# Kernel tuning notes

Measured on AMD Instinct MI355X. Metric: run time of the kernel, lower is better.

## Reference

```python
import jax, jax.numpy as jnp
import numpy as np

N = 100000
E = 1600000
IN = 256
H = 4
C = 64


def setup_inputs() -> dict:
    key = jax.random.key(0)
    k1, k2, k3, k4, k5, k6 = jax.random.split(key, 6)
    x = jax.random.normal(k1, (N, IN), dtype=jnp.float32)
    edge_index = jax.random.randint(k2, (2, E), 0, N, dtype=jnp.int64)
    W = jax.random.normal(k3, (IN, H * C), dtype=jnp.float32) * (1.0 / np.sqrt(IN))
    att_src = jax.random.normal(k4, (H, C), dtype=jnp.float32) * 0.1
    att_dst = jax.random.normal(k5, (H, C), dtype=jnp.float32) * 0.1
    bias = jax.random.normal(k6, (H * C,), dtype=jnp.float32) * 0.01
    return {"x": x, "edge_index": edge_index, "W": W, "att_src": att_src, "att_dst": att_dst, "bias": bias}


def reference(x, edge_index, W, att_src, att_dst, bias):
    n = x.shape[0]
    # PyG GATConv default: add self-loops
    loops = jnp.arange(n, dtype=edge_index.dtype)
    src = jnp.concatenate([edge_index[0], loops])  # [E+N]
    dst = jnp.concatenate([edge_index[1], loops])  # [E+N]
    xp = (x @ W).reshape(n, H, C)                   # [N,H,C]
    a_src = jnp.einsum('nhc,hc->nh', xp, att_src)   # [N,H]
    a_dst = jnp.einsum('nhc,hc->nh', xp, att_dst)   # [N,H]
    # per-edge attention logits, LeakyReLU(0.2)
    alpha = jax.nn.leaky_relu(a_src[src] + a_dst[dst], negative_slope=0.2)  # [E+N,H]
    # segment softmax over destination neighborhoods (every node has a self-loop)
    amax = jax.ops.segment_max(alpha, dst, num_segments=n)
    amax = jnp.where(jnp.isfinite(amax), amax, 0.0)
    ex = jnp.exp(alpha - amax[dst])
    denom = jax.ops.segment_sum(ex, dst, num_segments=n)
    w = ex / denom[dst]                              # [E+N,H]
    # weighted scatter-add of source features
    msg = xp[src] * w[..., None]                     # [E+N,H,C]
    agg = jax.ops.segment_sum(msg, dst, num_segments=n)  # [N,H,C]
    out = agg.reshape(n, H * C) + bias
    return jax.nn.elu(out)
```

## Files before the change

### kernel.cpp

```cpp
#include <hip/hip_runtime.h>
#include <hip/hip_fp16.h>

#define FDIM 256
#define NH 4

typedef float f32x4 __attribute__((ext_vector_type(4)));
typedef int   i32x4 __attribute__((ext_vector_type(4)));
typedef short short8v __attribute__((ext_vector_type(8)));
typedef unsigned short ushort_t;
typedef unsigned short ushort8 __attribute__((ext_vector_type(8)));
typedef unsigned short ushort4v __attribute__((ext_vector_type(4)));

__device__ __forceinline__ float leaky02(float v) { return v > 0.0f ? v : 0.2f * v; }

__device__ __forceinline__ ushort_t f2bf(float f) {
    union { float f; unsigned int u; } v; v.f = f;
    unsigned int u = v.u + 0x7FFFu + ((v.u >> 16) & 1u);
    return (ushort_t)(u >> 16);
}

__device__ __forceinline__ float bf2f(ushort_t u) {
    union { float f; unsigned int u; } v;
    v.u = ((unsigned int)u) << 16;
    return v.f;
}

__device__ __forceinline__ void gload_lds16(const void* g, void* lds) {
    __builtin_amdgcn_global_load_lds((const __attribute__((address_space(1))) unsigned int*)g,
                                     (__attribute__((address_space(3))) unsigned int*)lds, 16, 0, 0);
}

__device__ __forceinline__ float recw(const i32x4& r, int h) {
    unsigned v = (h < 2) ? (unsigned)r.y : (unsigned)r.z;
    unsigned bits = (h & 1) ? (v >> 16) : (v & 0xFFFFu);
    __half_raw hr; hr.x = (unsigned short)bits;
    return __half2float(*reinterpret_cast<__half*>(&hr));
}

__global__ __launch_bounds__(256) void wprep_kernel(const float* __restrict__ W,
                                                    ushort_t* __restrict__ Wbf) {
    const int k = blockIdx.x;
    const int col = threadIdx.x;
    Wbf[(((size_t)(k >> 3) * 256 + col) << 3) + (k & 7)] = f2bf(W[(size_t)k * 256 + col]);
}

__global__ __launch_bounds__(512) void gemm_xp_kernel(const float* __restrict__ x,
                                                      const ushort_t* __restrict__ Wbf,
                                                      const float* __restrict__ att_s,
                                                      const float* __restrict__ att_d,
                                                      ushort_t* __restrict__ xpb,
                                                      float* __restrict__ a_src,
                                                      float* __restrict__ a_dst, int n,
                                                      const int* __restrict__ dst,
                                                      int* __restrict__ counts, int E) {
    __shared__ ushort_t a_lds[4096];
    __shared__ ushort_t b_lds[8192];
    const int t = threadIdx.x;

    {
        const int per = (E + gridDim.x - 1) / gridDim.x;
        const int lo = blockIdx.x * per;
        const int hi = min(lo + per, E);
        for (int e = lo + t; e < hi; e += 512)
            atomicAdd(&counts[__builtin_nontemporal_load(&dst[e])], 1);
    }

    const int w = t >> 6, l = t & 63;
    const int wm = w >> 2, wn = w & 3;
    const int row0 = blockIdx.x << 7;
    const int fr = l & 15, fk = l >> 4;

    const int arow = t & 127, akb = t >> 7;
    int grow = row0 + arow;
    if (grow >= n) grow = n - 1;
    const float* aptr = x + (size_t)grow * FDIM + (akb << 3);

    f32x4 acc[4][4] = {};

    for (int s = 0; s < 8; ++s) {
        float4 v0 = *(const float4*)(aptr + s * 32);
        float4 v1 = *(const float4*)(aptr + s * 32 + 4);
        ushort8 u;
        u[0]=f2bf(v0.x); u[1]=f2bf(v0.y); u[2]=f2bf(v0.z); u[3]=f2bf(v0.w);
        u[4]=f2bf(v1.x); u[5]=f2bf(v1.y); u[6]=f2bf(v1.z); u[7]=f2bf(v1.w);

        if (s) __syncthreads();

        *(ushort8*)&a_lds[(((size_t)akb << 7) + arow) << 3] = u;
        gload_lds16(Wbf + (size_t)s * 8192 + ((size_t)t << 3), (char*)b_lds + (w << 10));
        gload_lds16(Wbf + (size_t)s * 8192 + ((size_t)(t + 512) << 3), (char*)b_lds + 8192 + (w << 10));
        __syncthreads();

        short8v af[4], bfv[4];
        #pragma unroll
        for (int m = 0; m < 4; ++m)
            af[m] = *(const short8v*)&a_lds[(((size_t)fk << 7) + wm * 64 + m * 16 + fr) << 3];
        #pragma unroll
        for (int nf = 0; nf < 4; ++nf)
            bfv[nf] = *(const short8v*)&b_lds[(((size_t)fk << 8) + wn * 64 + nf * 16 + fr) << 3];
        #pragma unroll
        for (int m = 0; m < 4; ++m)
            #pragma unroll
            for (int nf = 0; nf < 4; ++nf)
                acc[m][nf] = __builtin_amdgcn_mfma_f32_16x16x32_bf16(af[m], bfv[nf], acc[m][nf], 0, 0, 0);
    }

    #pragma unroll
    for (int m = 0; m < 4; ++m) {
        const int r_ = row0 + wm * 64 + m * 16 + fk * 4;
        #pragma unroll
        for (int nf = 0; nf < 4; ++nf) {
            const int c_ = wn * 64 + nf * 16 + fr;
            #pragma unroll
            for (int j = 0; j < 4; ++j)
                if (r_ + j < n)
                    xpb[(size_t)(r_ + j) * FDIM + c_] = f2bf(acc[m][nf][j]);
        }
    }

    float att_sv[4], att_dv[4];
    #pragma unroll
    for (int nf = 0; nf < 4; ++nf) {
        att_sv[nf] = att_s[(wn << 6) + (nf << 4) + fr];
        att_dv[nf] = att_d[(wn << 6) + (nf << 4) + fr];
    }
    #pragma unroll
    for (int m = 0; m < 4; ++m) {
        #pragma unroll
        for (int j = 0; j < 4; ++j) {
            float ps = acc[m][0][j] * att_sv[0] + acc[m][1][j] * att_sv[1]
                     + acc[m][2][j] * att_sv[2] + acc[m][3][j] * att_sv[3];
            float pd = acc[m][0][j] * att_dv[0] + acc[m][1][j] * att_dv[1]
                     + acc[m][2][j] * att_dv[2] + acc[m][3][j] * att_dv[3];
            ps += __shfl_xor(ps, 1, 64); pd += __shfl_xor(pd, 1, 64);
            ps += __shfl_xor(ps, 2, 64); pd += __shfl_xor(pd, 2, 64);
            ps += __shfl_xor(ps, 4, 64); pd += __shfl_xor(pd, 4, 64);
            ps += __shfl_xor(ps, 8, 64); pd += __shfl_xor(pd, 8, 64);
            if (fr == 0) {
                const int r_ = row0 + wm * 64 + m * 16 + fk * 4 + j;
                if (r_ < n) {
                    a_src[r_ * NH + wn] = ps;
                    a_dst[r_ * NH + wn] = pd;
                }
            }
        }
    }
}

__global__ __launch_bounds__(256) void scan_partial_kernel(const int* __restrict__ counts,
                                                           int* __restrict__ blockSums, int n) {
    __shared__ int sdata[256];
    const int b = blockIdx.x, t = threadIdx.x;
    const int base = b * 1024 + t * 4;
    int s = 0;
    #pragma unroll
    for (int j = 0; j < 4; ++j)
        if (base + j < n) s += counts[base + j];
    sdata[t] = s;
    __syncthreads();
    for (int off = 128; off > 0; off >>= 1) {
        if (t < off) sdata[t] += sdata[t + off];
        __syncthreads();
    }
    if (t == 0) blockSums[b] = sdata[0];
}

__global__ __launch_bounds__(256) void scan_final_kernel(const int* __restrict__ counts,
                                                         const int* __restrict__ blockSums,
                                                         int* __restrict__ offsets,
                                                         int* __restrict__ cursor, int n, int nb) {
    __shared__ int s[256];
    __shared__ int bs[256];
    const int b = blockIdx.x, t = threadIdx.x;
    int bv = (t < nb) ? blockSums[t] : 0;
    bs[t] = bv;
    __syncthreads();
    for (int d = 1; d < 256; d <<= 1) {
        int u = (t >= d) ? bs[t - d] : 0;
        __syncthreads();
        bs[t] += u;
        __syncthreads();
    }
    const int blockOff = (b > 0) ? bs[b - 1] : 0;

    const int base = b * 1024 + t * 4;
    int c[4];
    int tsum = 0;
    #pragma unroll
    for (int j = 0; j < 4; ++j) {
        c[j] = (base + j < n) ? counts[base + j] : 0;
        tsum += c[j];
    }
    s[t] = tsum;
    __syncthreads();
    for (int d = 1; d < 256; d <<= 1) {
        int u = (t >= d) ? s[t - d] : 0;
        __syncthreads();
        s[t] += u;
        __syncthreads();
    }
    int run = s[t] - tsum + blockOff;
    #pragma unroll
    for (int j = 0; j < 4; ++j) {
        if (base + j < n) {
            offsets[base + j] = run;
            cursor[base + j] = run;
            run += c[j];
        }
    }
}

__global__ void scatter_kernel(const int* __restrict__ src, const int* __restrict__ dst,
                               const float* __restrict__ a_src, const float* __restrict__ a_dst,
                               int* __restrict__ cursor, i32x4* __restrict__ erec, int E) {
    int stride = gridDim.x * blockDim.x;
    for (int e = blockIdx.x * blockDim.x + threadIdx.x; e < E; e += stride) {
        const int s = __builtin_nontemporal_load(&src[e]);
        const int d = __builtin_nontemporal_load(&dst[e]);
        const float4 as = ((const float4*)a_src)[s];
        const float4 ad = ((const float4*)a_dst)[d];
        const float w0 = __expf(leaky02(as.x + ad.x));
        const float w1 = __expf(leaky02(as.y + ad.y));
        const float w2 = __expf(leaky02(as.z + ad.z));
        const float w3 = __expf(leaky02(as.w + ad.w));
        union { __half2 h; int i; } p01, p23;
        p01.h = __floats2half2_rn(w0, w1);
        p23.h = __floats2half2_rn(w2, w3);
        i32x4 rec;
        rec.x = s; rec.y = p01.i; rec.z = p23.i; rec.w = 0;
        const int pos = atomicAdd(&cursor[d], 1);
        __builtin_nontemporal_store(rec, &erec[pos]);
    }
}

__global__ __launch_bounds__(256) void aggregate_kernel(const ushort_t* __restrict__ xpb,
                                                        const float* __restrict__ a_src,
                                                        const float* __restrict__ a_dst,
                                                        const int* __restrict__ offsets,
                                                        const int* __restrict__ counts,
                                                        const i32x4* __restrict__ erec,
                                                        const float* __restrict__ bias,
                                                        float* __restrict__ out, int n) {
    const int i = (blockIdx.x << 2) + (threadIdx.x >> 6);
    if (i >= n) return;
    const int lane = threadIdx.x & 63;
    const int halfid = lane >> 5, sl = lane & 31;
    const int h = sl >> 3;
    const size_t colb = (size_t)sl << 3;
    const int start = offsets[i];
    const int cnt = counts[i];
    const i32x4* recs = erec + start;

    float acc[8] = {};
    float den = 0.f;

    int e = 0;
    for (; e + 4 <= cnt; e += 4) {
        const i32x4 ra = recs[e + halfid];
        const i32x4 rb = recs[e + 2 + halfid];
        const ushort8 ua = *(const ushort8*)(xpb + (size_t)ra.x * FDIM + colb);
        const ushort8 ub = *(const ushort8*)(xpb + (size_t)rb.x * FDIM + colb);
        const float wa = recw(ra, h), wb = recw(rb, h);
        den += wa + wb;
        #pragma unroll
        for (int j = 0; j < 8; ++j) acc[j] = fmaf(wa, bf2f(ua[j]), acc[j]);
        #pragma unroll
        for (int j = 0; j < 8; ++j) acc[j] = fmaf(wb, bf2f(ub[j]), acc[j]);
    }
    for (; e < cnt; e += 2) {
        const int idx = e + halfid;
        const int cidx = idx < cnt ? idx : cnt - 1;
        const i32x4 r = recs[cidx];
        const ushort8 u = *(const ushort8*)(xpb + (size_t)r.x * FDIM + colb);
        const float wv = idx < cnt ? recw(r, h) : 0.f;
        den += wv;
        #pragma unroll
        for (int j = 0; j < 8; ++j) acc[j] = fmaf(wv, bf2f(u[j]), acc[j]);
    }
    if (halfid == 0) {
        const float ws = __expf(leaky02(a_src[i * NH + h] + a_dst[i * NH + h]));
        const ushort8 u = *(const ushort8*)(xpb + (size_t)i * FDIM + colb);
        den += ws;
        #pragma unroll
        for (int j = 0; j < 8; ++j) acc[j] = fmaf(ws, bf2f(u[j]), acc[j]);
    }
    den += __shfl_xor(den, 32, 64);
    #pragma unroll
    for (int j = 0; j < 8; ++j) acc[j] += __shfl_xor(acc[j], 32, 64);

    const float inv = 1.0f / den;
    const int c0 = (sl << 3) + (halfid << 2);
    const float4 b4 = *(const float4*)(bias + c0);
    const int jb = halfid << 2;
    f32x4 v;
    v.x = acc[jb + 0] * inv + b4.x;
    v.y = acc[jb + 1] * inv + b4.y;
    v.z = acc[jb + 2] * inv + b4.z;
    v.w = acc[jb + 3] * inv + b4.w;
    v.x = v.x > 0.f ? v.x : (__expf(v.x) - 1.f);
    v.y = v.y > 0.f ? v.y : (__expf(v.y) - 1.f);
    v.z = v.z > 0.f ? v.z : (__expf(v.z) - 1.f);
    v.w = v.w > 0.f ? v.w : (__expf(v.w) - 1.f);
    *(f32x4*)(out + (size_t)i * FDIM + c0) = v;
}

extern "C" void kernel_launch(void* const* d_in, const int* in_sizes, int n_in,
                              void* d_out, int out_size, void* d_ws, size_t ws_size,
                              hipStream_t stream) {
    const float* x       = (const float*)d_in[0];
    const int*   ei      = (const int*)d_in[1];
    const float* W       = (const float*)d_in[2];
    const float* att_s   = (const float*)d_in[3];
    const float* att_d   = (const float*)d_in[4];
    const float* bias    = (const float*)d_in[5];
    float* out = (float*)d_out;

    const int n = in_sizes[0] / FDIM;
    const int E = in_sizes[1] / 2;
    const int* src = ei;
    const int* dst = ei + E;

    char* ws = (char*)d_ws;
    size_t off = 0;
    auto alloc = [&](size_t bytes) -> void* {
        void* p = ws + off;
        off = (off + bytes + 255) & ~(size_t)255;
        return p;
    };
    ushort_t* xpb  = (ushort_t*)alloc((size_t)n * FDIM * sizeof(ushort_t));
    float* a_src   = (float*)alloc((size_t)n * NH * sizeof(float));
    float* a_dst   = (float*)alloc((size_t)n * NH * sizeof(float));
    int* counts    = (int*)alloc((size_t)n * sizeof(int));
    int* offsets   = (int*)alloc((size_t)n * sizeof(int));
    int* cursor    = (int*)alloc((size_t)n * sizeof(int));
    int* blockSums = (int*)alloc(256 * sizeof(int));
    i32x4* erec    = (i32x4*)alloc((size_t)E * sizeof(i32x4));
    ushort_t* Wbf  = (ushort_t*)alloc((size_t)FDIM * FDIM * sizeof(ushort_t));
    (void)ws_size;

    hipMemsetAsync(counts, 0, (size_t)n * sizeof(int), stream);

    wprep_kernel<<<256, 256, 0, stream>>>(W, Wbf);
    gemm_xp_kernel<<<(n + 127) / 128, 512, 0, stream>>>(x, Wbf, att_s, att_d, xpb, a_src, a_dst, n,
                                                        dst, counts, E);
    const int nb = (n + 1023) / 1024;
    scan_partial_kernel<<<nb, 256, 0, stream>>>(counts, blockSums, n);
    scan_final_kernel<<<nb, 256, 0, stream>>>(counts, blockSums, offsets, cursor, n, nb);
    scatter_kernel<<<2048, 256, 0, stream>>>(src, dst, a_src, a_dst, cursor, erec, E);
    aggregate_kernel<<<(n + 3) / 4, 256, 0, stream>>>(xpb, a_src, a_dst, offsets, counts, erec, bias, out, n);
}
```

Baseline: 340.0 us.

## Split GEMM over column halves, preload A tile, double-buffer W, separate degree count

The degree-count atomics move out of the GEMM into their own kernel. The GEMM now uses a 2D grid with 128-column tiles and 256 threads. The whole 128x256 A tile is converted to bf16 and loaded into LDS once, and the W slices are double-buffered through global_load_lds so the next slice's load overlaps the current MFMAs. The erec store in scatter also becomes a regular store instead of nontemporal. The trade-off is that x rows are read twice (once per column half), LDS use per block is larger, and there is one extra kernel launch.

```diff
diff --git a/kernel.cpp b/kernel.cpp
--- a/kernel.cpp
+++ b/kernel.cpp
@@ -9,7 +9,6 @@
 typedef short short8v __attribute__((ext_vector_type(8)));
 typedef unsigned short ushort_t;
 typedef unsigned short ushort8 __attribute__((ext_vector_type(8)));
-typedef unsigned short ushort4v __attribute__((ext_vector_type(4)));
 
 __device__ __forceinline__ float leaky02(float v) { return v > 0.0f ? v : 0.2f * v; }
 
@@ -44,65 +43,81 @@
     Wbf[(((size_t)(k >> 3) * 256 + col) << 3) + (k & 7)] = f2bf(W[(size_t)k * 256 + col]);
 }
 
-__global__ __launch_bounds__(512) void gemm_xp_kernel(const float* __restrict__ x,
+__global__ __launch_bounds__(256) void degree_kernel(const int* __restrict__ dst,
+                                                     int* __restrict__ counts, int E) {
+    int stride = gridDim.x * blockDim.x;
+    for (int e = blockIdx.x * blockDim.x + threadIdx.x; e < E; e += stride)
+        atomicAdd(&counts[dst[e]], 1);
+}
+
+__global__ __launch_bounds__(256) void gemm_xp_kernel(const float* __restrict__ x,
                                                       const ushort_t* __restrict__ Wbf,
                                                       const float* __restrict__ att_s,
                                                       const float* __restrict__ att_d,
                                                       ushort_t* __restrict__ xpb,
                                                       float* __restrict__ a_src,
-                                                      float* __restrict__ a_dst, int n,
-                                                      const int* __restrict__ dst,
-                                                      int* __restrict__ counts, int E) {
-    __shared__ ushort_t a_lds[4096];
-    __shared__ ushort_t b_lds[8192];
+                                                      float* __restrict__ a_dst, int n) {
+    __shared__ ushort_t a_lds[32 * 128 * 8];
+    __shared__ ushort_t b_lds[2][4 * 128 * 8];
     const int t = threadIdx.x;
-
-    {
-        const int per = (E + gridDim.x - 1) / gridDim.x;
-        const int lo = blockIdx.x * per;
-        const int hi = min(lo + per, E);
-        for (int e = lo + t; e < hi; e += 512)
-            atomicAdd(&counts[__builtin_nontemporal_load(&dst[e])], 1);
-    }
-
     const int w = t >> 6, l = t & 63;
-    const int wm = w >> 2, wn = w & 3;
+    const int wm = w >> 1, wn = w & 1;
     const int row0 = blockIdx.x << 7;
+    const int n0 = blockIdx.y << 7;
     const int fr = l & 15, fk = l >> 4;
 
-    const int arow = t & 127, akb = t >> 7;
+    auto stageB = [&](int s, int buf) {
+        #pragma unroll
+        for (int j = 0; j < 2; ++j) {
+            const int v = ((w << 1) + j) * 64 + l;
+            const ushort_t* g = Wbf + (((size_t)((s << 2) + (v >> 7)) << 8) + n0 + (v & 127)) * 8;
+            gload_lds16(g, (char*)b_lds + buf * 8192 + ((w << 1) + j) * 1024);
+        }
+    };
+    stageB(0, 0);
+
+    const int arow = t >> 1;
+    const int acol0 = (t & 1) << 7;
     int grow = row0 + arow;
     if (grow >= n) grow = n - 1;
-    const float* aptr = x + (size_t)grow * FDIM + (akb << 3);
+    const float* aptr = x + (size_t)grow * FDIM + acol0;
+
+    #pragma unroll
+    for (int vly = 0; vly < 2; ++vly) {
+        float4 av[16];
+        #pragma unroll
+        for (int q = 0; q < 16; ++q)
+            av[q] = *(const float4*)(aptr + vly * 64 + q * 4);
+        #pragma unroll
+        for (int g = 0; g < 8; ++g) {
+            ushort8 u;
+            u[0] = f2bf(av[2*g].x);   u[1] = f2bf(av[2*g].y);
+            u[2] = f2bf(av[2*g].z);   u[3] = f2bf(av[2*g].w);
+            u[4] = f2bf(av[2*g+1].x); u[5] = f2bf(av[2*g+1].y);
+            u[6] = f2bf(av[2*g+1].z); u[7] = f2bf(av[2*g+1].w);
+            const int kblk = ((acol0 + vly * 64) >> 3) + g;
+            *(ushort8*)&a_lds[(((size_t)kblk << 7) + arow) << 3] = u;
+        }
+    }
+    __syncthreads();
 
     f32x4 acc[4][4] = {};
-
     for (int s = 0; s < 8; ++s) {
-        float4 v0 = *(const float4*)(aptr + s * 32);
-        float4 v1 = *(const float4*)(aptr + s * 32 + 4);
-        ushort8 u;
-        u[0]=f2bf(v0.x); u[1]=f2bf(v0.y); u[2]=f2bf(v0.z); u[3]=f2bf(v0.w);
-        u[4]=f2bf(v1.x); u[5]=f2bf(v1.y); u[6]=f2bf(v1.z); u[7]=f2bf(v1.w);
-
-        if (s) __syncthreads();
-
-        *(ushort8*)&a_lds[(((size_t)akb << 7) + arow) << 3] = u;
-        gload_lds16(Wbf + (size_t)s * 8192 + ((size_t)t << 3), (char*)b_lds + (w << 10));
-        gload_lds16(Wbf + (size_t)s * 8192 + ((size_t)(t + 512) << 3), (char*)b_lds + 8192 + (w << 10));
-        __syncthreads();
-
+        const int buf = s & 1;
+        if (s < 7) stageB(s + 1, buf ^ 1);
         short8v af[4], bfv[4];
         #pragma unroll
         for (int m = 0; m < 4; ++m)
-            af[m] = *(const short8v*)&a_lds[(((size_t)fk << 7) + wm * 64 + m * 16 + fr) << 3];
+            af[m] = *(const short8v*)&a_lds[(((size_t)((s << 2) + fk) << 7) + wm * 64 + m * 16 + fr) << 3];
         #pragma unroll
         for (int nf = 0; nf < 4; ++nf)
-            bfv[nf] = *(const short8v*)&b_lds[(((size_t)fk << 8) + wn * 64 + nf * 16 + fr) << 3];
+            bfv[nf] = *(const short8v*)&b_lds[buf][(((size_t)fk << 7) + wn * 64 + nf * 16 + fr) << 3];
         #pragma unroll
         for (int m = 0; m < 4; ++m)
             #pragma unroll
             for (int nf = 0; nf < 4; ++nf)
                 acc[m][nf] = __builtin_amdgcn_mfma_f32_16x16x32_bf16(af[m], bfv[nf], acc[m][nf], 0, 0, 0);
+        if (s < 7) __syncthreads();
     }
 
     #pragma unroll
@@ -110,7 +125,7 @@
         const int r_ = row0 + wm * 64 + m * 16 + fk * 4;
         #pragma unroll
         for (int nf = 0; nf < 4; ++nf) {
-            const int c_ = wn * 64 + nf * 16 + fr;
+            const int c_ = n0 + wn * 64 + nf * 16 + fr;
             #pragma unroll
             for (int j = 0; j < 4; ++j)
                 if (r_ + j < n)
@@ -118,11 +133,12 @@
         }
     }
 
+    const int h = (n0 >> 6) + wn;
     float att_sv[4], att_dv[4];
     #pragma unroll
     for (int nf = 0; nf < 4; ++nf) {
-        att_sv[nf] = att_s[(wn << 6) + (nf << 4) + fr];
-        att_dv[nf] = att_d[(wn << 6) + (nf << 4) + fr];
+        att_sv[nf] = att_s[(h << 6) + (nf << 4) + fr];
+        att_dv[nf] = att_d[(h << 6) + (nf << 4) + fr];
     }
     #pragma unroll
     for (int m = 0; m < 4; ++m) {
@@ -139,8 +155,8 @@
             if (fr == 0) {
                 const int r_ = row0 + wm * 64 + m * 16 + fk * 4 + j;
                 if (r_ < n) {
-                    a_src[r_ * NH + wn] = ps;
-                    a_dst[r_ * NH + wn] = pd;
+                    a_src[r_ * NH + h] = ps;
+                    a_dst[r_ * NH + h] = pd;
                 }
             }
         }
@@ -229,7 +245,7 @@
         i32x4 rec;
         rec.x = s; rec.y = p01.i; rec.z = p23.i; rec.w = 0;
         const int pos = atomicAdd(&cursor[d], 1);
-        __builtin_nontemporal_store(rec, &erec[pos]);
+        erec[pos] = rec;
     }
 }
 
@@ -341,11 +357,13 @@
     hipMemsetAsync(counts, 0, (size_t)n * sizeof(int), stream);
 
     wprep_kernel<<<256, 256, 0, stream>>>(W, Wbf);
-    gemm_xp_kernel<<<(n + 127) / 128, 512, 0, stream>>>(x, Wbf, att_s, att_d, xpb, a_src, a_dst, n,
-                                                        dst, counts, E);
+    degree_kernel<<<2048, 256, 0, stream>>>(dst, counts, E);
+    dim3 gg((n + 127) / 128, 2);
+    gemm_xp_kernel<<<gg, 256, 0, stream>>>(x, Wbf, att_s, att_d, xpb, a_src, a_dst, n);
     const int nb = (n + 1023) / 1024;
     scan_partial_kernel<<<nb, 256, 0, stream>>>(counts, blockSums, n);
     scan_final_kernel<<<nb, 256, 0, stream>>>(counts, blockSums, offsets, cursor, n, nb);
     scatter_kernel<<<2048, 256, 0, stream>>>(src, dst, a_src, a_dst, cursor, erec, E);
-    aggregate_kernel<<<(n + 3) / 4, 256, 0, stream>>>(xpb, a_src, a_dst, offsets, counts, erec, bias, out, n);
-}
+    aggregate_kernel<<<(n + 3) / 4, 256, 0, stream>>>(xpb, a_src, a_dst, offsets, counts, erec,
+                                                      bias, out, n);
+}
```

Measured after the change: 376.3 us. 1.11x slower.

## Preload full A tile, double-buffer W stages, and stage GEMM output through LDS

Applied to the files above, without the earlier changes.

The GEMM kernel now loads the whole 128x256 x tile up front, using coalesced float4 loads with padded LDS rows. It double-buffers the bf16 W chunks so the next chunk loads while the current MFMA step runs, which removes one barrier per k-step. Output xp is written through a swizzled LDS tile so global stores become 16-byte coalesced rows instead of scattered 2-byte stores. The scatter kernel's nontemporal store of edge records becomes a plain store. The larger LDS footprint (about 98KB) and 64 float4 registers per thread may lower occupancy.

```diff
diff --git a/kernel.cpp b/kernel.cpp
--- a/kernel.cpp
+++ b/kernel.cpp
@@ -44,6 +44,7 @@
     Wbf[(((size_t)(k >> 3) * 256 + col) << 3) + (k & 7)] = f2bf(W[(size_t)k * 256 + col]);
 }
 
+#define AKP 1032
 __global__ __launch_bounds__(512) void gemm_xp_kernel(const float* __restrict__ x,
                                                       const ushort_t* __restrict__ Wbf,
                                                       const float* __restrict__ att_s,
@@ -53,8 +54,8 @@
                                                       float* __restrict__ a_dst, int n,
                                                       const int* __restrict__ dst,
                                                       int* __restrict__ counts, int E) {
-    __shared__ ushort_t a_lds[4096];
-    __shared__ ushort_t b_lds[8192];
+    __shared__ ushort_t a_sm[32 * AKP];
+    __shared__ ushort_t b_sm[2][8192];
     const int t = threadIdx.x;
 
     {
@@ -70,52 +71,83 @@
     const int row0 = blockIdx.x << 7;
     const int fr = l & 15, fk = l >> 4;
 
-    const int arow = t & 127, akb = t >> 7;
-    int grow = row0 + arow;
-    if (grow >= n) grow = n - 1;
-    const float* aptr = x + (size_t)grow * FDIM + (akb << 3);
+    auto stageB = [&](int s, int buf) {
+        #pragma unroll
+        for (int j = 0; j < 2; ++j) {
+            const int c = (w << 1) + j;
+            const int kb = c >> 2, half = c & 3;
+            const ushort_t* g = Wbf + (((size_t)((s << 2) + kb) << 8) + (half << 6) + l) * 8;
+            gload_lds16(g, (char*)&b_sm[buf][0] + kb * 4096 + half * 1024);
+        }
+    };
+    stageB(0, 0);
+
+    const int c64 = t & 63;
+    const int r0t = t >> 6;
+    float4 av[16];
+    #pragma unroll
+    for (int q = 0; q < 16; ++q) {
+        int gr = row0 + r0t + 8 * q;
+        if (gr >= n) gr = n - 1;
+        av[q] = *(const float4*)(x + (size_t)gr * FDIM + (c64 << 2));
+    }
+    const int akb = c64 >> 1, aoff = (c64 & 1) << 2;
+    #pragma unroll
+    for (int q = 0; q < 16; ++q) {
+        ushort4v u;
+        u[0] = f2bf(av[q].x); u[1] = f2bf(av[q].y);
+        u[2] = f2bf(av[q].z); u[3] = f2bf(av[q].w);
+        *(ushort4v*)&a_sm[(size_t)akb * AKP + (size_t)(r0t + 8 * q) * 8 + aoff] = u;
+    }
+    __syncthreads();
 
     f32x4 acc[4][4] = {};
-
     for (int s = 0; s < 8; ++s) {
-        float4 v0 = *(const float4*)(aptr + s * 32);
-        float4 v1 = *(const float4*)(aptr + s * 32 + 4);
-        ushort8 u;
-        u[0]=f2bf(v0.x); u[1]=f2bf(v0.y); u[2]=f2bf(v0.z); u[3]=f2bf(v0.w);
-        u[4]=f2bf(v1.x); u[5]=f2bf(v1.y); u[6]=f2bf(v1.z); u[7]=f2bf(v1.w);
-
-        if (s) __syncthreads();
-
-        *(ushort8*)&a_lds[(((size_t)akb << 7) + arow) << 3] = u;
-        gload_lds16(Wbf + (size_t)s * 8192 + ((size_t)t << 3), (char*)b_lds + (w << 10));
-        gload_lds16(Wbf + (size_t)s * 8192 + ((size_t)(t + 512) << 3), (char*)b_lds + 8192 + (w << 10));
-        __syncthreads();
-
+        const int buf = s & 1;
+        if (s < 7) stageB(s + 1, buf ^ 1);
         short8v af[4], bfv[4];
         #pragma unroll
         for (int m = 0; m < 4; ++m)
-            af[m] = *(const short8v*)&a_lds[(((size_t)fk << 7) + wm * 64 + m * 16 + fr) << 3];
+            af[m] = *(const short8v*)&a_sm[(size_t)((s << 2) + fk) * AKP
+                                           + (size_t)(wm * 64 + m * 16 + fr) * 8];
         #pragma unroll
         for (int nf = 0; nf < 4; ++nf)
-            bfv[nf] = *(const short8v*)&b_lds[(((size_t)fk << 8) + wn * 64 + nf * 16 + fr) << 3];
+            bfv[nf] = *(const short8v*)&b_sm[buf][((fk << 8) + wn * 64 + nf * 16 + fr) << 3];
         #pragma unroll
         for (int m = 0; m < 4; ++m)
             #pragma unroll
             for (int nf = 0; nf < 4; ++nf)
                 acc[m][nf] = __builtin_amdgcn_mfma_f32_16x16x32_bf16(af[m], bfv[nf], acc[m][nf], 0, 0, 0);
-    }
-
+        if (s < 7) __syncthreads();
+    }
+    __syncthreads();
+
+    ushort_t* c_lds = a_sm;
     #pragma unroll
     for (int m = 0; m < 4; ++m) {
-        const int r_ = row0 + wm * 64 + m * 16 + fk * 4;
         #pragma unroll
         for (int nf = 0; nf < 4; ++nf) {
-            const int c_ = wn * 64 + nf * 16 + fr;
+            const int col = wn * 64 + nf * 16 + fr;
             #pragma unroll
-            for (int j = 0; j < 4; ++j)
-                if (r_ + j < n)
-                    xpb[(size_t)(r_ + j) * FDIM + c_] = f2bf(acc[m][nf][j]);
+            for (int j = 0; j < 4; ++j) {
+                const int row = wm * 64 + m * 16 + fk * 4 + j;
+                const int colS = col ^ (((row >> 2) & 3) << 4);
+                c_lds[row * 256 + colS] = f2bf(acc[m][nf][j]);
+            }
         }
+    }
+    __syncthreads();
+
+    #pragma unroll
+    for (int q = 0; q < 8; ++q) {
+        const int idx = t + 512 * q;
+        const int row = idx >> 5;
+        const int cblk = idx & 31;
+        const int cblkS = cblk ^ (((row >> 2) & 3) << 1);
+        const ushort8 u = *(const ushort8*)&c_lds[row * 256 + cblkS * 8];
+        const int gr = row0 + row;
+        if (gr < n)
+            *(ushort8*)(xpb + (size_t)gr * FDIM + (cblk << 3)) = u;
     }
 
     float att_sv[4], att_dv[4];
@@ -229,7 +261,7 @@
         i32x4 rec;
         rec.x = s; rec.y = p01.i; rec.z = p23.i; rec.w = 0;
         const int pos = atomicAdd(&cursor[d], 1);
-        __builtin_nontemporal_store(rec, &erec[pos]);
+        erec[pos] = rec;
     }
 }
 
@@ -347,5 +379,6 @@
     scan_partial_kernel<<<nb, 256, 0, stream>>>(counts, blockSums, n);
     scan_final_kernel<<<nb, 256, 0, stream>>>(counts, blockSums, offsets, cursor, n, nb);
     scatter_kernel<<<2048, 256, 0, stream>>>(src, dst, a_src, a_dst, cursor, erec, E);
-    aggregate_kernel<<<(n + 3) / 4, 256, 0, stream>>>(xpb, a_src, a_dst, offsets, counts, erec, bias, out, n);
-}
+    aggregate_kernel<<<(n + 3) / 4, 256, 0, stream>>>(xpb, a_src, a_dst, offsets, counts, erec,
+                                                      bias, out, n);
+}
```

New measurement: 356.9 us. 5.0% more time.
